# Performance work log

Measured on AMD Instinct MI355X. Metric: run time of the kernel, lower is better.

The kernel has to match this reference:

```python
import jax, jax.numpy as jnp
import numpy as np

N_NODES = 50000
N_EDGES = 800000
D_FEAT = 64
N_AGENTS = 1024
A_DIM = 16
MSG = 128          # msg_dim
OUT = 128          # out_dim


def _w(k, fan_in, fan_out):
    return jax.random.normal(k, (fan_in, fan_out), jnp.float32) / np.sqrt(fan_in).astype(np.float32)


def setup_inputs() -> dict:
    key = jax.random.key(0)
    ks = jax.random.split(key, 24)
    inp = {}
    inp["x"] = jax.random.normal(ks[0], (N_NODES, D_FEAT), jnp.float32)
    inp["actions"] = jax.random.normal(ks[1], (N_AGENTS, A_DIM), jnp.float32)
    inp["senders"] = jax.random.randint(ks[2], (N_EDGES,), 0, N_NODES, jnp.int32)
    inp["receivers"] = jax.random.randint(ks[3], (N_EDGES,), 0, N_NODES, jnp.int32)
    inp["n_agents"] = N_AGENTS
    # message MLP: concat(sender, receiver) -> 256 -> 256 -> msg_dim
    inp["W_m1"] = _w(ks[4], 2 * D_FEAT, 256); inp["b_m1"] = jnp.zeros((256,), jnp.float32)
    inp["W_m2"] = _w(ks[5], 256, 256);        inp["b_m2"] = jnp.zeros((256,), jnp.float32)
    inp["W_m3"] = _w(ks[6], 256, MSG);        inp["b_m3"] = jnp.zeros((MSG,), jnp.float32)
    # aggregation MLP: msg_dim -> 128 -> 128 -> msg_dim
    inp["W_a1"] = _w(ks[7], MSG, 128);        inp["b_a1"] = jnp.zeros((128,), jnp.float32)
    inp["W_a2"] = _w(ks[8], 128, 128);        inp["b_a2"] = jnp.zeros((128,), jnp.float32)
    inp["W_a3"] = _w(ks[9], 128, MSG);        inp["b_a3"] = jnp.zeros((MSG,), jnp.float32)
    # update MLP: concat(node, aggregated) -> 256 -> 256 -> out_dim
    inp["W_u1"] = _w(ks[10], D_FEAT + MSG, 256); inp["b_u1"] = jnp.zeros((256,), jnp.float32)
    inp["W_u2"] = _w(ks[11], 256, 256);          inp["b_u2"] = jnp.zeros((256,), jnp.float32)
    inp["W_u3"] = _w(ks[12], 256, OUT);          inp["b_u3"] = jnp.zeros((OUT,), jnp.float32)
    # critic head
    inp["W_act"] = _w(ks[13], A_DIM, 128);    inp["b_act"] = jnp.zeros((128,), jnp.float32)
    inp["W_h1"] = _w(ks[14], OUT + 128, 256); inp["b_h1"] = jnp.zeros((256,), jnp.float32)
    inp["W_h2"] = _w(ks[15], 256, 256);       inp["b_h2"] = jnp.zeros((256,), jnp.float32)
    inp["W_q"] = _w(ks[16], 256, 1);          inp["b_q"] = jnp.zeros((1,), jnp.float32)
    return inp


def reference(x, actions, senders, receivers, n_agents,
              W_m1, b_m1, W_m2, b_m2, W_m3, b_m3,
              W_a1, b_a1, W_a2, b_a2, W_a3, b_a3,
              W_u1, b_u1, W_u2, b_u2, W_u3, b_u3,
              W_act, b_act, W_h1, b_h1, W_h2, b_h2, W_q, b_q):
    relu = jax.nn.relu
    # --- GNN layer: edge messages (gather endpoints, MLP) ---
    h = jnp.concatenate([x[senders], x[receivers]], axis=-1)   # [E, 2*D]
    h = relu(h @ W_m1 + b_m1)
    h = relu(h @ W_m2 + b_m2)
    msg = h @ W_m3 + b_m3                                      # [E, MSG]
    # --- aggregate messages at receivers (scatter-add) ---
    aggr = jax.ops.segment_sum(msg, receivers, num_segments=x.shape[0])  # [N, MSG]
    a = relu(aggr @ W_a1 + b_a1)
    a = relu(a @ W_a2 + b_a2)
    a = a @ W_a3 + b_a3                                        # [N, MSG]
    # --- node update ---
    u = jnp.concatenate([x, a], axis=-1)                       # [N, D+MSG]
    u = relu(u @ W_u1 + b_u1)
    u = relu(u @ W_u2 + b_u2)
    feats = (u @ W_u3 + b_u3)[:n_agents]                       # agent (type-0) nodes
    # --- critic head ---
    ap = relu(actions @ W_act + b_act)                         # [n_agents, 128]
    z = jnp.concatenate([feats, ap], axis=-1)
    z = relu(z @ W_h1 + b_h1)
    z = relu(z @ W_h2 + b_h2)
    q = z @ W_q + b_q
    return jnp.squeeze(q, axis=-1)                             # [n_agents]
```

## Files before the change

kernel.cpp:

```cpp
#include <hip/hip_runtime.h>


#define STRIDE 260

#define FILT_CHUNK 4096
__global__ void filter_edges(const int* __restrict__ senders,
                             const int* __restrict__ receivers,
                             int E, int n_agents, int cap,
                             int* __restrict__ counter, int2* __restrict__ edges) {
    __shared__ int lcount;
    __shared__ int lbase;
    __shared__ int2 lbuf[FILT_CHUNK];
    const int t = (int)threadIdx.x;
    if (t == 0) lcount = 0;
    __syncthreads();
    int start = blockIdx.x * FILT_CHUNK;
    int end = min(start + FILT_CHUNK, E);
    for (int b0 = start; b0 < end; b0 += 256) {
        int idx = b0 + t;
        int r = -1, s = 0;
        bool pred = false;
        if (idx < end) {
            r = receivers[idx];
            pred = (r < n_agents);
            if (pred) s = senders[idx];
        }
        unsigned long long m = __ballot(pred);
        int lane = t & 63;
        int below = __popcll(m & ((1ull << lane) - 1));
        int cnt = __popcll(m);
        int wbase = 0;
        if (lane == 0 && cnt) wbase = atomicAdd(&lcount, cnt);
        wbase = __shfl(wbase, 0, 64);
        if (pred) lbuf[wbase + below] = make_int2(s, r);
    }
    __syncthreads();
    if (t == 0) lbase = atomicAdd(counter, lcount);
    __syncthreads();
    for (int i = t; i < lcount; i += 256) {
        int pos = lbase + i;
        if (pos < cap) edges[pos] = lbuf[i];
    }
}

template<int TE, int NIN, int NOUT, int COLS, int KS, bool RELU, int OOFF, int UNR>
__device__ __forceinline__ void mlp_layer(const float* in_lds, float* out_lds,
                                          float* part_lds,
                                          const float* __restrict__ W,
                                          const float* __restrict__ b) {
    constexpr int TX = NOUT / COLS;
    constexpr int NG = 256 / TX;
    static_assert(NG % KS == 0, "k-splits divide groups");
    constexpr int RG = NG / KS;
    static_assert(TE % RG == 0, "rows divide row-groups");
    constexpr int ER = TE / RG;
    constexpr int KRANGE = NIN / KS;
    static_assert(KRANGE % 4 == 0, "k-range multiple of 4");

    const int t   = (int)threadIdx.x;
    const int tx  = t % TX;
    const int grp = t / TX;
    const int ks  = grp % KS;
    const int rg  = grp / KS;
    const int o   = tx * COLS;
    const int e0  = rg * ER;
    const int k0  = ks * KRANGE;

    float acc[ER][COLS];
#pragma unroll
    for (int er = 0; er < ER; ++er)
#pragma unroll
        for (int c = 0; c < COLS; ++c) acc[er][c] = 0.f;

#pragma unroll UNR
    for (int kb = 0; kb < KRANGE; kb += 4) {
        const int k = k0 + kb;
        float w[4][COLS];
#pragma unroll
        for (int j = 0; j < 4; ++j) {
            const float* wp = W + (size_t)(k + j) * NOUT + o;
            if (COLS == 4) {
                float4 v = *(const float4*)wp;
                w[j][0] = v.x; w[j][1] = v.y; w[j][2] = v.z; w[j][3] = v.w;
            } else {
                float2 v = *(const float2*)wp;
                w[j][0] = v.x; w[j][1] = v.y;
            }
        }
#pragma unroll
        for (int er = 0; er < ER; ++er) {
            float4 a = *(const float4*)(in_lds + (e0 + er) * STRIDE + k);
#pragma unroll
            for (int c = 0; c < COLS; ++c) {
                acc[er][c] += a.x * w[0][c] + a.y * w[1][c]
                            + a.z * w[2][c] + a.w * w[3][c];
            }
        }
    }

    if (KS == 1) {
#pragma unroll
        for (int er = 0; er < ER; ++er) {
            float v[COLS];
#pragma unroll
            for (int c = 0; c < COLS; ++c) {
                v[c] = acc[er][c] + b[o + c];
                if (RELU) v[c] = fmaxf(v[c], 0.f);
            }
            float* dst = out_lds + (e0 + er) * STRIDE + OOFF + o;
            if (COLS == 4) *(float4*)dst = make_float4(v[0], v[1], v[2], v[3]);
            else           *(float2*)dst = make_float2(v[0], v[1]);
        }
    } else {
        if (ks != 0) {
            float* pr = (ks == 1) ? out_lds : part_lds + (size_t)(ks - 2) * TE * STRIDE;
#pragma unroll
            for (int er = 0; er < ER; ++er) {
                float* dst = pr + (e0 + er) * STRIDE + OOFF + o;
                if (COLS == 4) *(float4*)dst = make_float4(acc[er][0], acc[er][1],
                                                           acc[er][2], acc[er][3]);
                else           *(float2*)dst = make_float2(acc[er][0], acc[er][1]);
            }
        }
        __syncthreads();
        if (ks == 0) {
#pragma unroll
            for (int er = 0; er < ER; ++er) {
                float v[COLS];
#pragma unroll
                for (int c = 0; c < COLS; ++c) v[c] = acc[er][c];
#pragma unroll
                for (int j = 1; j < KS; ++j) {
                    const float* pr = (j == 1) ? out_lds
                                               : part_lds + (size_t)(j - 2) * TE * STRIDE;
                    const float* src = pr + (e0 + er) * STRIDE + OOFF + o;
                    if (COLS == 4) {
                        float4 p = *(const float4*)src;
                        v[0] += p.x; v[1] += p.y; v[2] += p.z; v[3] += p.w;
                    } else {
                        float2 p = *(const float2*)src;
                        v[0] += p.x; v[1] += p.y;
                    }
                }
#pragma unroll
                for (int c = 0; c < COLS; ++c) {
                    v[c] += b[o + c];
                    if (RELU) v[c] = fmaxf(v[c], 0.f);
                }
                float* dst = out_lds + (e0 + er) * STRIDE + OOFF + o;
                if (COLS == 4) *(float4*)dst = make_float4(v[0], v[1], v[2], v[3]);
                else           *(float2*)dst = make_float2(v[0], v[1]);
            }
        }
    }
}

#define ETE 32
__global__ __launch_bounds__(256, 2)
void edge_mlp(const float* __restrict__ x, const int2* __restrict__ edges,
              const int* __restrict__ counter, int cap, float* __restrict__ aggr,
              const float* __restrict__ Wm1, const float* __restrict__ bm1,
              const float* __restrict__ Wm2, const float* __restrict__ bm2,
              const float* __restrict__ Wm3, const float* __restrict__ bm3) {
    __shared__ float bufA[ETE * STRIDE];
    __shared__ float bufB[ETE * STRIDE];
    __shared__ int sL[ETE], rL[ETE];
    const int count = min(counter[0], cap);
    const int ntiles = (count + ETE - 1) / ETE;
    const int t = (int)threadIdx.x;
    for (int tile = (int)blockIdx.x; tile < ntiles; tile += (int)gridDim.x) {
        const int base = tile * ETE;
        if (t < ETE) {
            int eg = base + t;
            int2 ed = (eg < count) ? edges[eg] : make_int2(0, -1);
            sL[t] = ed.x; rL[t] = ed.y;
        }
        __syncthreads();
        for (int idx = t; idx < ETE * 32; idx += 256) {
            int e = idx >> 5;
            int f4 = (idx & 31) * 4;
            int node = (f4 < 64) ? sL[e] : rL[e];
            float4 v = make_float4(0.f, 0.f, 0.f, 0.f);
            if (rL[e] >= 0) v = *(const float4*)(x + (size_t)node * 64 + (f4 & 63));
            *(float4*)(bufA + e * STRIDE + f4) = v;
        }
        __syncthreads();
        mlp_layer<ETE, 128, 256, 4, 2, true,  0, 2>(bufA, bufB, nullptr, Wm1, bm1);
        __syncthreads();
        mlp_layer<ETE, 256, 256, 4, 2, true,  0, 2>(bufB, bufA, nullptr, Wm2, bm2);
        __syncthreads();
        mlp_layer<ETE, 256, 128, 4, 2, false, 0, 2>(bufA, bufB, nullptr, Wm3, bm3);
        __syncthreads();
        for (int idx = t; idx < ETE * 128; idx += 256) {
            int e = idx >> 7, o = idx & 127;
            if (base + e < count) {
                atomicAdd(&aggr[(size_t)rL[e] * 128 + o], bufB[e * STRIDE + o]);
            }
        }
        __syncthreads();
    }
}

#define NTE 4
__global__ __launch_bounds__(256, 1)
void node_update(const float* __restrict__ x, const float* __restrict__ actions,
                 const float* __restrict__ aggr, int n_agents,
                 const float* __restrict__ Wa1, const float* __restrict__ ba1,
                 const float* __restrict__ Wa2, const float* __restrict__ ba2,
                 const float* __restrict__ Wa3, const float* __restrict__ ba3,
                 const float* __restrict__ Wu1, const float* __restrict__ bu1,
                 const float* __restrict__ Wu2, const float* __restrict__ bu2,
                 const float* __restrict__ Wu3, const float* __restrict__ bu3,
                 const float* __restrict__ Wact, const float* __restrict__ bact,
                 const float* __restrict__ Wh1, const float* __restrict__ bh1,
                 const float* __restrict__ Wh2, const float* __restrict__ bh2,
                 const float* __restrict__ Wq,  const float* __restrict__ bq,
                 float* __restrict__ out) {
    __shared__ float bufA[NTE * STRIDE];
    __shared__ float bufB[NTE * STRIDE];
    __shared__ float bufP[2 * NTE * STRIDE];
    const int t = (int)threadIdx.x;
    const int base = (int)blockIdx.x * NTE;

    if (t < NTE * 32) {
        int e = t >> 5, f4 = (t & 31) * 4;
        int node = base + e;
        float4 v = make_float4(0.f, 0.f, 0.f, 0.f);
        if (node < n_agents) v = *(const float4*)(aggr + (size_t)node * 128 + f4);
        *(float4*)(bufA + e * STRIDE + f4) = v;
    }
    __syncthreads();
    mlp_layer<NTE, 128, 128, 2, 4, true,  0, 8>(bufA, bufB, bufP, Wa1, ba1); __syncthreads();
    mlp_layer<NTE, 128, 128, 2, 4, true,  0, 8>(bufB, bufA, bufP, Wa2, ba2); __syncthreads();
    mlp_layer<NTE, 128, 128, 2, 4, false, 0, 8>(bufA, bufB, bufP, Wa3, ba3); __syncthreads();
    if (t < NTE * 16) {
        int e = t >> 4, f4 = (t & 15) * 4;
        int node = base + e;
        float4 v = make_float4(0.f, 0.f, 0.f, 0.f);
        if (node < n_agents) v = *(const float4*)(x + (size_t)node * 64 + f4);
        *(float4*)(bufA + e * STRIDE + f4) = v;
    }
    if (t < NTE * 32) {
        int e = t >> 5, f4 = (t & 31) * 4;
        *(float4*)(bufA + e * STRIDE + 64 + f4) = *(const float4*)(bufB + e * STRIDE + f4);
    }
    __syncthreads();
    mlp_layer<NTE, 192, 256, 4, 4, true,  0, 4>(bufA, bufB, bufP, Wu1, bu1); __syncthreads();
    mlp_layer<NTE, 256, 256, 4, 4, true,  0, 4>(bufB, bufA, bufP, Wu2, bu2); __syncthreads();
    mlp_layer<NTE, 256, 128, 2, 4, false, 0, 4>(bufA, bufB, bufP, Wu3, bu3); __syncthreads();
    if (t < NTE * 4) {
        int e = t >> 2, f4 = (t & 3) * 4;
        int node = base + e;
        float4 v = make_float4(0.f, 0.f, 0.f, 0.f);
        if (node < n_agents) v = *(const float4*)(actions + (size_t)node * 16 + f4);
        *(float4*)(bufA + e * STRIDE + f4) = v;
    }
    __syncthreads();
    mlp_layer<NTE, 16,  128, 2, 4, true, 128, 1>(bufA, bufB, bufP, Wact, bact); __syncthreads();
    mlp_layer<NTE, 256, 256, 4, 4, true, 0,   4>(bufB, bufA, bufP, Wh1, bh1); __syncthreads();
    mlp_layer<NTE, 256, 256, 4, 4, true, 0,   4>(bufA, bufB, bufP, Wh2, bh2); __syncthreads();
    {
        int wv = t >> 6, lane = t & 63;
        int node = base + wv;
        float4 z = *(const float4*)(bufB + wv * STRIDE + lane * 4);
        float4 qw = *(const float4*)(Wq + lane * 4);
        float p = z.x * qw.x + z.y * qw.y + z.z * qw.z + z.w * qw.w;
#pragma unroll
        for (int off = 32; off >= 1; off >>= 1) p += __shfl_down(p, off, 64);
        if (lane == 0 && node < n_agents) out[node] = p + bq[0];
    }
}

extern "C" void kernel_launch(void* const* d_in, const int* in_sizes, int n_in,
                              void* d_out, int out_size, void* d_ws, size_t ws_size,
                              hipStream_t stream) {
    const float* x        = (const float*)d_in[0];
    const float* actions  = (const float*)d_in[1];
    const int*   senders  = (const int*)d_in[2];
    const int*   receivers= (const int*)d_in[3];
    const float* Wm1 = (const float*)d_in[5],  *bm1 = (const float*)d_in[6];
    const float* Wm2 = (const float*)d_in[7],  *bm2 = (const float*)d_in[8];
    const float* Wm3 = (const float*)d_in[9],  *bm3 = (const float*)d_in[10];
    const float* Wa1 = (const float*)d_in[11], *ba1 = (const float*)d_in[12];
    const float* Wa2 = (const float*)d_in[13], *ba2 = (const float*)d_in[14];
    const float* Wa3 = (const float*)d_in[15], *ba3 = (const float*)d_in[16];
    const float* Wu1 = (const float*)d_in[17], *bu1 = (const float*)d_in[18];
    const float* Wu2 = (const float*)d_in[19], *bu2 = (const float*)d_in[20];
    const float* Wu3 = (const float*)d_in[21], *bu3 = (const float*)d_in[22];
    const float* Wact= (const float*)d_in[23], *bact= (const float*)d_in[24];
    const float* Wh1 = (const float*)d_in[25], *bh1 = (const float*)d_in[26];
    const float* Wh2 = (const float*)d_in[27], *bh2 = (const float*)d_in[28];
    const float* Wq  = (const float*)d_in[29], *bq  = (const float*)d_in[30];

    const int E = in_sizes[2];
    const int n_agents = out_size;

    char* ws = (char*)d_ws;
    int*   counter = (int*)ws;
    float* aggr    = (float*)(ws + 1024);
    size_t aggrBytes = (size_t)n_agents * 128 * sizeof(float);
    size_t edgeOff = 1024 + ((aggrBytes + 1023) / 1024) * 1024;
    int2*  edges   = (int2*)(ws + edgeOff);
    int cap = (int)((ws_size > edgeOff) ? (ws_size - edgeOff) / sizeof(int2) : 0);
    if (cap > E) cap = E;

    hipMemsetAsync(ws, 0, edgeOff, stream);

    int fblocks = (E + FILT_CHUNK - 1) / FILT_CHUNK;
    filter_edges<<<fblocks, 256, 0, stream>>>(senders, receivers, E, n_agents,
                                              cap, counter, edges);

    edge_mlp<<<512, 256, 0, stream>>>(x, edges, counter, cap, aggr,
                                      Wm1, bm1, Wm2, bm2, Wm3, bm3);

    node_update<<<(n_agents + NTE - 1) / NTE, 256, 0, stream>>>(
        x, actions, aggr, n_agents,
        Wa1, ba1, Wa2, ba2, Wa3, ba3,
        Wu1, bu1, Wu2, bu2, Wu3, bu3,
        Wact, bact, Wh1, bh1, Wh2, bh2, Wq, bq,
        (float*)d_out);
}
```

Before: 240.2 us.

## Run edge MLP on bf16 MFMA with split-precision hi/lo weights

Replaces the scalar FP32 edge-MLP layers with MFMA 16x16x32 bf16 matrix instructions. Activations and weights are each split into bf16 hi and lo parts, and three MFMAs per tile approximate FP32 accuracy. A new pack_weights kernel converts the edge-MLP weights into the MFMA fragment layout in workspace on every call. The aim is to move the dominant edge GEMMs onto matrix cores, at the cost of an extra launch, conversion work inside the inner loop, and a small accuracy loss from the three-term split.

Result: faster. 198.5 us (-17.3%).

```diff
diff --git a/kernel.cpp b/kernel.cpp
--- a/kernel.cpp
+++ b/kernel.cpp
@@ -1,7 +1,64 @@
 #include <hip/hip_runtime.h>
+#include <hip/hip_bf16.h>
 
 
 #define STRIDE 260
+
+typedef __attribute__((ext_vector_type(8))) short short8;
+typedef __attribute__((ext_vector_type(4))) float floatx4;
+
+union Frag8 { short8 s; uint u[4]; };
+
+__device__ __forceinline__ void cvt_hi_lo(const float4 f0, const float4 f1,
+                                          Frag8& hi, Frag8& lo) {
+    uint U[8] = { __float_as_uint(f0.x), __float_as_uint(f0.y),
+                  __float_as_uint(f0.z), __float_as_uint(f0.w),
+                  __float_as_uint(f1.x), __float_as_uint(f1.y),
+                  __float_as_uint(f1.z), __float_as_uint(f1.w) };
+    float F[8] = { f0.x, f0.y, f0.z, f0.w, f1.x, f1.y, f1.z, f1.w };
+#pragma unroll
+    for (int p = 0; p < 4; ++p) {
+        uint a = U[2*p], b = U[2*p+1];
+        hi.u[p] = (a >> 16) | (b & 0xFFFF0000u);
+        float l0 = F[2*p]   - __uint_as_float(a & 0xFFFF0000u);
+        float l1 = F[2*p+1] - __uint_as_float(b & 0xFFFF0000u);
+        __hip_bfloat162 pl = __float22bfloat162_rn(make_float2(l0, l1));
+        union { __hip_bfloat162 h; uint v; } cvt; cvt.h = pl;
+        lo.u[p] = cvt.v;
+    }
+}
+
+__global__ void pack_weights(const float* __restrict__ Wm1,
+                             const float* __restrict__ Wm2,
+                             const float* __restrict__ Wm3,
+                             uint* __restrict__ pack) {
+    int g = blockIdx.x * 256 + threadIdx.x;
+    const float* W; int NOUT, NT, local; uint *dhi, *dlo;
+    if (g < 4096)       { W = Wm1; NOUT = 256; NT = 16; local = g;         dhi = pack;          dlo = pack + 16384; }
+    else if (g < 12288) { W = Wm2; NOUT = 256; NT = 16; local = g - 4096;  dhi = pack + 32768;  dlo = pack + 65536; }
+    else                { W = Wm3; NOUT = 128; NT = 8;  local = g - 12288; dhi = pack + 98304;  dlo = pack + 114688; }
+    int lane = local & 63;
+    int tmp  = local >> 6;
+    int nt = tmp % NT, kb = tmp / NT;
+    int n  = nt * 16 + (lane & 15);
+    int k0 = kb * 32 + ((lane >> 4) & 3) * 8;
+    uint hi[4], lo[4];
+#pragma unroll
+    for (int p = 0; p < 4; ++p) {
+        float f0 = W[(size_t)(k0 + 2*p)     * NOUT + n];
+        float f1 = W[(size_t)(k0 + 2*p + 1) * NOUT + n];
+        uint U0 = __float_as_uint(f0), U1 = __float_as_uint(f1);
+        hi[p] = (U0 >> 16) | (U1 & 0xFFFF0000u);
+        float l0 = f0 - __uint_as_float(U0 & 0xFFFF0000u);
+        float l1 = f1 - __uint_as_float(U1 & 0xFFFF0000u);
+        __hip_bfloat162 pl = __float22bfloat162_rn(make_float2(l0, l1));
+        union { __hip_bfloat162 h; uint v; } cvt; cvt.h = pl;
+        lo[p] = cvt.v;
+    }
+    int idx = ((kb * NT + nt) * 64 + lane) * 4;
+    *(uint4*)(dhi + idx) = make_uint4(hi[0], hi[1], hi[2], hi[3]);
+    *(uint4*)(dlo + idx) = make_uint4(lo[0], lo[1], lo[2], lo[3]);
+}
 
 #define FILT_CHUNK 4096
 __global__ void filter_edges(const int* __restrict__ senders,
@@ -40,6 +97,118 @@
     for (int i = t; i < lcount; i += 256) {
         int pos = lbase + i;
         if (pos < cap) edges[pos] = lbuf[i];
+    }
+}
+
+template<int NIN, int NOUT, bool RELU>
+__device__ __forceinline__ void mfma_layer(const float* in_lds, float* out_lds,
+                                           const uint4* __restrict__ Whi,
+                                           const uint4* __restrict__ Wlo,
+                                           const float* __restrict__ b) {
+    constexpr int KB  = NIN / 32;
+    constexpr int NT  = NOUT / 16;
+    constexpr int NTW = NT / 4;
+    const int t    = (int)threadIdx.x;
+    const int wave = t >> 6;
+    const int l15  = t & 15;
+    const int quad = (t >> 4) & 3;
+
+    floatx4 acc[2][NTW];
+#pragma unroll
+    for (int mt = 0; mt < 2; ++mt)
+#pragma unroll
+        for (int i = 0; i < NTW; ++i) acc[mt][i] = (floatx4){0.f, 0.f, 0.f, 0.f};
+
+#pragma unroll 2
+    for (int kb = 0; kb < KB; ++kb) {
+        Frag8 ahi[2], alo[2];
+#pragma unroll
+        for (int mt = 0; mt < 2; ++mt) {
+            const float* src = in_lds + (mt * 16 + l15) * STRIDE + kb * 32 + quad * 8;
+            float4 f0 = *(const float4*)src;
+            float4 f1 = *(const float4*)(src + 4);
+            cvt_hi_lo(f0, f1, ahi[mt], alo[mt]);
+        }
+#pragma unroll
+        for (int i = 0; i < NTW; ++i) {
+            int nt = wave * NTW + i;
+            int widx = (kb * NT + nt) * 64 + (t & 63);
+            Frag8 bhi, blo;
+            *(uint4*)bhi.u = Whi[widx];
+            *(uint4*)blo.u = Wlo[widx];
+#pragma unroll
+            for (int mt = 0; mt < 2; ++mt) {
+                acc[mt][i] = __builtin_amdgcn_mfma_f32_16x16x32_bf16(alo[mt].s, bhi.s, acc[mt][i], 0, 0, 0);
+                acc[mt][i] = __builtin_amdgcn_mfma_f32_16x16x32_bf16(ahi[mt].s, blo.s, acc[mt][i], 0, 0, 0);
+                acc[mt][i] = __builtin_amdgcn_mfma_f32_16x16x32_bf16(ahi[mt].s, bhi.s, acc[mt][i], 0, 0, 0);
+            }
+        }
+    }
+#pragma unroll
+    for (int i = 0; i < NTW; ++i) {
+        int n = (wave * NTW + i) * 16 + l15;
+        float bias = b[n];
+#pragma unroll
+        for (int mt = 0; mt < 2; ++mt) {
+#pragma unroll
+            for (int r = 0; r < 4; ++r) {
+                float v = acc[mt][i][r] + bias;
+                if (RELU) v = fmaxf(v, 0.f);
+                out_lds[(mt * 16 + quad * 4 + r) * STRIDE + n] = v;
+            }
+        }
+    }
+}
+
+#define ETE 32
+__global__ __launch_bounds__(256, 2)
+void edge_mlp(const float* __restrict__ x, const int2* __restrict__ edges,
+              const int* __restrict__ counter, int cap, float* __restrict__ aggr,
+              const uint* __restrict__ pack,
+              const float* __restrict__ bm1, const float* __restrict__ bm2,
+              const float* __restrict__ bm3) {
+    __shared__ float bufA[ETE * STRIDE];
+    __shared__ float bufB[ETE * STRIDE];
+    __shared__ int sL[ETE], rL[ETE];
+    const uint4* W1hi = (const uint4*)(pack);
+    const uint4* W1lo = (const uint4*)(pack + 16384);
+    const uint4* W2hi = (const uint4*)(pack + 32768);
+    const uint4* W2lo = (const uint4*)(pack + 65536);
+    const uint4* W3hi = (const uint4*)(pack + 98304);
+    const uint4* W3lo = (const uint4*)(pack + 114688);
+    const int count = min(counter[0], cap);
+    const int ntiles = (count + ETE - 1) / ETE;
+    const int t = (int)threadIdx.x;
+    for (int tile = (int)blockIdx.x; tile < ntiles; tile += (int)gridDim.x) {
+        const int base = tile * ETE;
+        if (t < ETE) {
+            int eg = base + t;
+            int2 ed = (eg < count) ? edges[eg] : make_int2(0, -1);
+            sL[t] = ed.x; rL[t] = ed.y;
+        }
+        __syncthreads();
+        for (int idx = t; idx < ETE * 32; idx += 256) {
+            int e = idx >> 5;
+            int f4 = (idx & 31) * 4;
+            int node = (f4 < 64) ? sL[e] : rL[e];
+            float4 v = make_float4(0.f, 0.f, 0.f, 0.f);
+            if (rL[e] >= 0) v = *(const float4*)(x + (size_t)node * 64 + (f4 & 63));
+            *(float4*)(bufA + e * STRIDE + f4) = v;
+        }
+        __syncthreads();
+        mfma_layer<128, 256, true >(bufA, bufB, W1hi, W1lo, bm1);
+        __syncthreads();
+        mfma_layer<256, 256, true >(bufB, bufA, W2hi, W2lo, bm2);
+        __syncthreads();
+        mfma_layer<256, 128, false>(bufA, bufB, W3hi, W3lo, bm3);
+        __syncthreads();
+        for (int idx = t; idx < ETE * 128; idx += 256) {
+            int e = idx >> 7, o = idx & 127;
+            if (base + e < count) {
+                atomicAdd(&aggr[(size_t)rL[e] * 128 + o], bufB[e * STRIDE + o]);
+            }
+        }
+        __syncthreads();
     }
 }
 
@@ -152,52 +321,6 @@
                 else           *(float2*)dst = make_float2(v[0], v[1]);
             }
         }
-    }
-}
-
-#define ETE 32
-__global__ __launch_bounds__(256, 2)
-void edge_mlp(const float* __restrict__ x, const int2* __restrict__ edges,
-              const int* __restrict__ counter, int cap, float* __restrict__ aggr,
-              const float* __restrict__ Wm1, const float* __restrict__ bm1,
-              const float* __restrict__ Wm2, const float* __restrict__ bm2,
-              const float* __restrict__ Wm3, const float* __restrict__ bm3) {
-    __shared__ float bufA[ETE * STRIDE];
-    __shared__ float bufB[ETE * STRIDE];
-    __shared__ int sL[ETE], rL[ETE];
-    const int count = min(counter[0], cap);
-    const int ntiles = (count + ETE - 1) / ETE;
-    const int t = (int)threadIdx.x;
-    for (int tile = (int)blockIdx.x; tile < ntiles; tile += (int)gridDim.x) {
-        const int base = tile * ETE;
-        if (t < ETE) {
-            int eg = base + t;
-            int2 ed = (eg < count) ? edges[eg] : make_int2(0, -1);
-            sL[t] = ed.x; rL[t] = ed.y;
-        }
-        __syncthreads();
-        for (int idx = t; idx < ETE * 32; idx += 256) {
-            int e = idx >> 5;
-            int f4 = (idx & 31) * 4;
-            int node = (f4 < 64) ? sL[e] : rL[e];
-            float4 v = make_float4(0.f, 0.f, 0.f, 0.f);
-            if (rL[e] >= 0) v = *(const float4*)(x + (size_t)node * 64 + (f4 & 63));
-            *(float4*)(bufA + e * STRIDE + f4) = v;
-        }
-        __syncthreads();
-        mlp_layer<ETE, 128, 256, 4, 2, true,  0, 2>(bufA, bufB, nullptr, Wm1, bm1);
-        __syncthreads();
-        mlp_layer<ETE, 256, 256, 4, 2, true,  0, 2>(bufB, bufA, nullptr, Wm2, bm2);
-        __syncthreads();
-        mlp_layer<ETE, 256, 128, 4, 2, false, 0, 2>(bufA, bufB, nullptr, Wm3, bm3);
-        __syncthreads();
-        for (int idx = t; idx < ETE * 128; idx += 256) {
-            int e = idx >> 7, o = idx & 127;
-            if (base + e < count) {
-                atomicAdd(&aggr[(size_t)rL[e] * 128 + o], bufB[e * STRIDE + o]);
-            }
-        }
-        __syncthreads();
     }
 }
 
@@ -298,20 +421,23 @@
     char* ws = (char*)d_ws;
     int*   counter = (int*)ws;
     float* aggr    = (float*)(ws + 1024);
-    size_t aggrBytes = (size_t)n_agents * 128 * sizeof(float);
-    size_t edgeOff = 1024 + ((aggrBytes + 1023) / 1024) * 1024;
+    const size_t packOff = 1024 + (size_t)n_agents * 128 * sizeof(float);
+    uint*  pack    = (uint*)(ws + packOff);
+    const size_t edgeOff = packOff + 524288;
     int2*  edges   = (int2*)(ws + edgeOff);
     int cap = (int)((ws_size > edgeOff) ? (ws_size - edgeOff) / sizeof(int2) : 0);
     if (cap > E) cap = E;
 
-    hipMemsetAsync(ws, 0, edgeOff, stream);
+    hipMemsetAsync(ws, 0, packOff, stream);
+
+    pack_weights<<<64, 256, 0, stream>>>(Wm1, Wm2, Wm3, pack);
 
     int fblocks = (E + FILT_CHUNK - 1) / FILT_CHUNK;
     filter_edges<<<fblocks, 256, 0, stream>>>(senders, receivers, E, n_agents,
                                               cap, counter, edges);
 
-    edge_mlp<<<512, 256, 0, stream>>>(x, edges, counter, cap, aggr,
-                                      Wm1, bm1, Wm2, bm2, Wm3, bm3);
+    edge_mlp<<<512, 256, 0, stream>>>(x, edges, counter, cap, aggr, pack,
+                                      bm1, bm2, bm3);
 
     node_update<<<(n_agents + NTE - 1) / NTE, 256, 0, stream>>>(
         x, actions, aggr, n_agents,
```
